# Kernel optimization log

Measured on AMD Instinct MI355X. Metric: run time of the kernel, lower is better.

## Reference

```python
import jax, jax.numpy as jnp
import numpy as np
from jax import lax

N_NEURONS = 2500
K = 50
T = 60
F = 5
H = 128
GROUP_SIZES = [800, 700, 600, 400]  # support_resistance, trend, pattern, volume
GID = jnp.asarray(np.repeat(np.arange(4), GROUP_SIZES))  # [N] specialty id per neuron
_BOUNDS = np.cumsum([0] + GROUP_SIZES)


def _lstm_layer(x, w_ih, w_hh, b_ih, b_hh):
    # x: [B,T,in]; PyTorch gate order i,f,g,o in the 4H weight rows
    B = x.shape[0]
    Hd = w_hh.shape[1]
    def step(carry, xt):
        h, c = carry
        g = xt @ w_ih.T + h @ w_hh.T + b_ih + b_hh
        i, f, gg, o = jnp.split(g, 4, axis=-1)
        c = jax.nn.sigmoid(f) * c + jax.nn.sigmoid(i) * jnp.tanh(gg)
        h = jax.nn.sigmoid(o) * jnp.tanh(c)
        return (h, c), h
    init = (jnp.zeros((B, Hd), x.dtype), jnp.zeros((B, Hd), x.dtype))
    (h, _), ys = lax.scan(step, init, jnp.swapaxes(x, 0, 1))
    return jnp.swapaxes(ys, 0, 1), h


def _forward(x, w_ih0, w_hh0, b_ih0, b_hh0, w_ih1, w_hh1, b_ih1, b_hh1,
             pw1, pb1, pw2, pb2, conn_w, sens, thr,
             iw1, ib1, iw2, ib2, iw3, ib3,
             hw_trend, hb_trend, hw_pat, hb_pat, hw_key, hb_key,
             hw_vol, hb_vol, hw_conf, hb_conf, conn_idx):
    seq, _ = _lstm_layer(x, w_ih0, w_hh0, b_ih0, b_hh0)
    _, h2 = _lstm_layer(seq, w_ih1, w_hh1, b_ih1, b_hh1)  # hidden[-1]: [B,H]
    # feature_projection: Linear->ReLU->Linear->Tanh
    base = jnp.tanh(jax.nn.relu(h2 @ pw1.T + pb1) @ pw2.T + pb2)  # [B,32]
    # broadcast base features to a per-neuron activation vector [B,N]
    reps = -(-N_NEURONS // base.shape[1])
    all_act = jnp.tile(base, (1, reps))[:, :N_NEURONS]
    # batched sparse gather + per-neuron weighted sum
    gathered = all_act[:, conn_idx]                       # [B,N,K]
    z = jnp.einsum('bnk,nk->bn', gathered, conn_w) * sens  # [B,N]
    # specialty-conditioned activation
    a = jnp.where(GID == 0, jax.nn.sigmoid(z - thr),
        jnp.where(GID == 1, jnp.tanh(z),
        jnp.where(GID == 2, jax.nn.relu(z - thr), jax.nn.sigmoid(z))))
    # integrator (dropout is eval-mode no-op)
    integ = jnp.tanh(jax.nn.relu(jax.nn.relu(a @ iw1.T + ib1) @ iw2.T + ib2) @ iw3.T + ib3)
    trend = integ @ hw_trend.T + hb_trend      # [B,3]
    pat = integ @ hw_pat.T + hb_pat            # [B,6]
    key_l = integ @ hw_key.T + hb_key          # [B,4]
    vol = integ @ hw_vol.T + hb_vol            # [B,1]
    conf = integ @ hw_conf.T + hb_conf         # [B,1]
    overall = jax.nn.sigmoid(conf)             # [B,1]
    means = jnp.stack([a[:, _BOUNDS[i]:_BOUNDS[i + 1]].mean(axis=1) for i in range(4)], axis=1)
    return jnp.concatenate([trend, pat, key_l, vol, conf, overall, means], axis=1)  # [B,20]


def setup_inputs() -> dict:
    key = jax.random.key(0)
    ks = iter(jax.random.split(key, 64))
    def rn(shape, s=0.05):
        return jax.random.normal(next(ks), shape, jnp.float32) * s
    B = 1024
    return {
        'x': jax.random.normal(next(ks), (B, T, F), jnp.float32),
        'conn_idx': jax.random.randint(next(ks), (N_NEURONS, K), 0, N_NEURONS, jnp.int32),
        'w_ih0': rn((4 * H, F)), 'w_hh0': rn((4 * H, H)),
        'b_ih0': rn((4 * H,), 0.01), 'b_hh0': rn((4 * H,), 0.01),
        'w_ih1': rn((4 * H, H)), 'w_hh1': rn((4 * H, H)),
        'b_ih1': rn((4 * H,), 0.01), 'b_hh1': rn((4 * H,), 0.01),
        'pw1': rn((64, H)), 'pb1': rn((64,), 0.01),
        'pw2': rn((32, 64)), 'pb2': rn((32,), 0.01),
        'conn_w': rn((N_NEURONS, K), 0.1),
        'sens': rn((N_NEURONS,), 0.1) + 1.0,
        'thr': rn((N_NEURONS,), 0.1) + 0.6,
        'iw1': rn((256, N_NEURONS), 0.01), 'ib1': rn((256,), 0.01),
        'iw2': rn((64, 256)), 'ib2': rn((64,), 0.01),
        'iw3': rn((32, 64)), 'ib3': rn((32,), 0.01),
        'hw_trend': rn((3, 32)), 'hb_trend': rn((3,), 0.01),
        'hw_pat': rn((6, 32)), 'hb_pat': rn((6,), 0.01),
        'hw_key': rn((4, 32)), 'hb_key': rn((4,), 0.01),
        'hw_vol': rn((1, 32)), 'hb_vol': rn((1,), 0.01),
        'hw_conf': rn((1, 32)), 'hb_conf': rn((1,), 0.01),
    }


def reference(x, conn_idx, w_ih0, w_hh0, b_ih0, b_hh0, w_ih1, w_hh1, b_ih1, b_hh1,
              pw1, pb1, pw2, pb2, conn_w, sens, thr,
              iw1, ib1, iw2, ib2, iw3, ib3,
              hw_trend, hb_trend, hw_pat, hb_pat, hw_key, hb_key,
              hw_vol, hb_vol, hw_conf, hb_conf):
    return _forward(x, w_ih0, w_hh0, b_ih0, b_hh0, w_ih1, w_hh1, b_ih1, b_hh1,
                    pw1, pb1, pw2, pb2, conn_w, sens, thr,
                    iw1, ib1, iw2, ib2, iw3, ib3,
                    hw_trend, hb_trend, hw_pat, hb_pat, hw_key, hb_key,
                    hw_vol, hb_vol, hw_conf, hb_conf, conn_idx)
```

## Files before the change

kernel.cpp:

```cpp
#include <hip/hip_runtime.h>
#include <hip/hip_bf16.h>
#include <math.h>

#define DEV __device__ __forceinline__

typedef short short8 __attribute__((ext_vector_type(8)));
typedef float f32x4  __attribute__((ext_vector_type(4)));

DEV float sigf(float x)   { return 1.0f / (1.0f + __expf(-x)); }
DEV float tanhft(float x) { return 1.0f - 2.0f / (__expf(2.0f * x) + 1.0f); }

DEV unsigned short f2bf(float f) {
    unsigned int u = __float_as_uint(f);
    unsigned int r = (u + 0x7FFFu + ((u >> 16) & 1u)) >> 16;
    return (unsigned short)r;
}
DEV float bf2f(unsigned short u) {
    return __uint_as_float(((unsigned int)u) << 16);
}

DEV void bar_lds() {
    asm volatile("s_waitcnt lgkmcnt(0)" ::: "memory");
    __builtin_amdgcn_s_barrier();
}

__global__ __launch_bounds__(256) void prep_kernel(
    const float* __restrict__ w_hh0, const float* __restrict__ w_ih1,
    const float* __restrict__ w_hh1,
    const float* __restrict__ b_ih0, const float* __restrict__ b_hh0,
    const float* __restrict__ b_ih1, const float* __restrict__ b_hh1,
    unsigned short* __restrict__ whh0h, unsigned short* __restrict__ wih1h,
    unsigned short* __restrict__ whh1h,
    float* __restrict__ bias0, float* __restrict__ bias1)
{
    int i = blockIdx.x * 256 + threadIdx.x;
    if (i < 65536) {
        whh0h[i] = f2bf(w_hh0[i]);
        wih1h[i] = f2bf(w_ih1[i]);
        whh1h[i] = f2bf(w_hh1[i]);
    } else if (i < 66048) {
        int c = i - 65536;
        bias0[c] = b_ih0[c] + b_hh0[c];
        bias1[c] = b_ih1[c] + b_hh1[c];
    }
}

__global__ __launch_bounds__(256) void prep_iw1_kernel(
    const float* __restrict__ iw1, unsigned short* __restrict__ iw1b)
{
    int i = blockIdx.x * 256 + threadIdx.x;
    if (i < 256 * 2528) {
        int row = i / 2528, k = i - row * 2528;
        iw1b[i] = (k < 2500) ? f2bf(iw1[row * 2500 + k]) : (unsigned short)0;
    }
}

__global__ __launch_bounds__(512, 2) void lstm_kernel(
    const float* __restrict__ x,
    const unsigned short* __restrict__ whh0,
    const unsigned short* __restrict__ wih1,
    const unsigned short* __restrict__ whh1,
    const float* __restrict__ wih0,
    const float* __restrict__ bias0, const float* __restrict__ bias1,
    float* __restrict__ h2out)
{
    __shared__ __align__(16) float          xs[4][304];
    __shared__ __align__(16) unsigned short h0s[2][16][136];
    __shared__ __align__(16) unsigned short h1s[2][16][136];
    __shared__ __align__(16) float          wsc[8][4][16][4];
    __shared__ float wih0s[2560];

    const int tid = threadIdx.x;
    const int b0  = blockIdx.x * 4;
    const int l15 = tid & 15;
    const int q   = (tid >> 4) & 3;
    const int w   = tid >> 6;
    const int j   = w * 16 + l15;
    const int q8  = q * 8;

    for (int i = tid; i < 1200; i += 512) {
        int m = i / 300, kk = i - m * 300;
        xs[m][kk] = x[(b0 + m) * 300 + kk];
    }
    for (int i = tid; i < 2560; i += 512) wih0s[i] = wih0[i];
    for (int i = tid; i < 2176; i += 512) {
        ((unsigned int*)h0s)[i] = 0u;
        ((unsigned int*)h1s)[i] = 0u;
    }

    float ub0[4], ub1[4];
#pragma unroll
    for (int g = 0; g < 4; ++g) {
        ub0[g] = bias0[g * 128 + j];
        ub1[g] = bias1[g * 128 + j];
    }

    short8 bh0[4][4], b1i[4][4];
#pragma unroll
    for (int g = 0; g < 4; ++g)
#pragma unroll
        for (int kc = 0; kc < 4; ++kc) {
            int off = (g * 128 + j) * 128 + kc * 32 + q8;
            bh0[g][kc] = *(const short8*)(whh0 + off);
            b1i[g][kc] = *(const short8*)(wih1 + off);
        }

    float c0 = 0.f, c1 = 0.f, hl = 0.f;
    __syncthreads();

    const unsigned short* wsb = whh1 + j * 128 + q8;

    for (int t = 0; t < 60; ++t) {
        const int p = t & 1;

        short8 wsv[4][4];
#pragma unroll
        for (int g = 0; g < 4; ++g) {
            wsv[g][0] = *(const short8*)(wsb + g * 16384);
            wsv[g][1] = *(const short8*)(wsb + g * 16384 + 32);
        }

        f32x4 acc[4];
#pragma unroll
        for (int g = 0; g < 4; ++g) acc[g] = (f32x4){0.f, 0.f, 0.f, 0.f};
        short8 af[4];
#pragma unroll
        for (int kc = 0; kc < 4; ++kc)
            af[kc] = *(const short8*)&h0s[p][l15][kc * 32 + q8];
#pragma unroll
        for (int kc = 0; kc < 4; ++kc)
#pragma unroll
            for (int g = 0; g < 4; ++g)
                acc[g] = __builtin_amdgcn_mfma_f32_16x16x32_bf16(af[kc], bh0[g][kc], acc[g], 0, 0, 0);

#pragma unroll
        for (int g = 0; g < 4; ++g) {
            wsv[g][2] = *(const short8*)(wsb + g * 16384 + 64);
            wsv[g][3] = *(const short8*)(wsb + g * 16384 + 96);
        }

        if (q == 0) {
#pragma unroll
            for (int g = 0; g < 4; ++g)
                *(f32x4*)&wsc[w][g][l15][0] = acc[g];
        }
        {
            const float* xr = &xs[q][t * 5];
            float x0 = xr[0], x1 = xr[1], x2 = xr[2], x3 = xr[3], x4 = xr[4];
            float gv[4];
#pragma unroll
            for (int g = 0; g < 4; ++g) {
                const float* wr = &wih0s[(g * 128 + j) * 5];
                float s = wsc[w][g][l15][q] + ub0[g];
                s = fmaf(x0, wr[0], s);
                s = fmaf(x1, wr[1], s);
                s = fmaf(x2, wr[2], s);
                s = fmaf(x3, wr[3], s);
                gv[g] = fmaf(x4, wr[4], s);
            }
            c0 = sigf(gv[1]) * c0 + sigf(gv[0]) * tanhft(gv[2]);
            float h = sigf(gv[3]) * tanhft(c0);
            h0s[1 - p][q][j] = f2bf(h);
        }

        bar_lds();

#pragma unroll
        for (int g = 0; g < 4; ++g) acc[g] = (f32x4){0.f, 0.f, 0.f, 0.f};
#pragma unroll
        for (int kc = 0; kc < 4; ++kc)
            af[kc] = *(const short8*)&h0s[1 - p][l15][kc * 32 + q8];
#pragma unroll
        for (int kc = 0; kc < 4; ++kc)
#pragma unroll
            for (int g = 0; g < 4; ++g)
                acc[g] = __builtin_amdgcn_mfma_f32_16x16x32_bf16(af[kc], b1i[g][kc], acc[g], 0, 0, 0);
#pragma unroll
        for (int kc = 0; kc < 4; ++kc)
            af[kc] = *(const short8*)&h1s[p][l15][kc * 32 + q8];
#pragma unroll
        for (int kc = 0; kc < 4; ++kc)
#pragma unroll
            for (int g = 0; g < 4; ++g)
                acc[g] = __builtin_amdgcn_mfma_f32_16x16x32_bf16(af[kc], wsv[g][kc], acc[g], 0, 0, 0);

        if (q == 0) {
#pragma unroll
            for (int g = 0; g < 4; ++g)
                *(f32x4*)&wsc[w][g][l15][0] = acc[g];
        }
        {
            float gv[4];
#pragma unroll
            for (int g = 0; g < 4; ++g)
                gv[g] = wsc[w][g][l15][q] + ub1[g];
            c1 = sigf(gv[1]) * c1 + sigf(gv[0]) * tanhft(gv[2]);
            float h = sigf(gv[3]) * tanhft(c1);
            h1s[1 - p][q][j] = f2bf(h);
            hl = h;
        }
    }

    h2out[(b0 + q) * 128 + j] = hl;
}

__global__ __launch_bounds__(64) void phase2_kernel(
    const float* __restrict__ h2, const float* __restrict__ pw1,
    const float* __restrict__ pb1, const float* __restrict__ pw2,
    const float* __restrict__ pb2, float* __restrict__ base)
{
    __shared__ float hs[128], p1[64];
    int b = blockIdx.x, tid = threadIdx.x;
    hs[tid] = h2[b * 128 + tid];
    hs[tid + 64] = h2[b * 128 + 64 + tid];
    __syncthreads();
    float acc = pb1[tid];
#pragma unroll 4
    for (int k = 0; k < 128; ++k) acc = fmaf(hs[k], pw1[tid * 128 + k], acc);
    p1[tid] = fmaxf(acc, 0.f);
    __syncthreads();
    if (tid < 32) {
        float a2 = pb2[tid];
#pragma unroll 4
        for (int k = 0; k < 64; ++k) a2 = fmaf(p1[k], pw2[tid * 64 + k], a2);
        base[b * 32 + tid] = tanhft(a2);
    }
}

__global__ __launch_bounds__(128) void weff_kernel(
    const int* __restrict__ conn_idx, const float* __restrict__ conn_w,
    float* __restrict__ weffT)
{
    __shared__ float s[128 * 33];
    int tid = threadIdx.x;
    int n = blockIdx.x * 128 + tid;
    float* sr = &s[tid * 33];
#pragma unroll
    for (int j = 0; j < 32; ++j) sr[j] = 0.f;
    if (n < 2500) {
        for (int k = 0; k < 50; ++k) {
            int idx = conn_idx[n * 50 + k];
            sr[idx & 31] += conn_w[n * 50 + k];
        }
        for (int j = 0; j < 32; ++j) weffT[j * 2500 + n] = sr[j];
    }
}

__global__ __launch_bounds__(256) void za_kernel(
    const float* __restrict__ base, const float* __restrict__ weffT,
    const float* __restrict__ sens, const float* __restrict__ thr,
    unsigned short* __restrict__ amat)
{
    __shared__ float bs[16][32];
    int tid = threadIdx.x;
    int bb = blockIdx.x / 10, nb = blockIdx.x % 10;
    int n = nb * 256 + tid;
    bool nv = n < 2500;
    bool pv = n < 2528;
    int nn = nv ? n : 0;
    for (int i = tid; i < 512; i += 256) bs[i >> 5][i & 31] = base[bb * 512 + i];
    __syncthreads();
    float w[32];
#pragma unroll
    for (int j = 0; j < 32; ++j) w[j] = weffT[j * 2500 + nn];
    float sn = sens[nn], tn = thr[nn];
    int g = (n < 800) ? 0 : (n < 1500) ? 1 : (n < 2100) ? 2 : 3;
#pragma unroll 2
    for (int r = 0; r < 16; ++r) {
        float z = 0.f;
#pragma unroll
        for (int j = 0; j < 32; ++j) z = fmaf(bs[r][j], w[j], z);
        z *= sn;
        float av;
        if (g == 0)      av = sigf(z - tn);
        else if (g == 1) av = tanhft(z);
        else if (g == 2) av = fmaxf(z - tn, 0.f);
        else             av = sigf(z);
        if (nv)      amat[(bb * 16 + r) * 2528 + n] = f2bf(av);
        else if (pv) amat[(bb * 16 + r) * 2528 + n] = 0;
    }
}

__global__ __launch_bounds__(128) void gemm_iw1_kernel(
    const unsigned short* __restrict__ ab, const unsigned short* __restrict__ wb,
    const float* __restrict__ ib1, float* __restrict__ t1)
{
    const int tid = threadIdx.x;
    const int wv  = tid >> 6;
    const int l15 = tid & 15, q = (tid >> 4) & 3, q8 = q * 8;
    const int row0 = blockIdx.y * 32 + wv * 16;
    const int col0 = blockIdx.x * 64;

    const unsigned short* A = ab + (row0 + l15) * 2528 + q8;
    const unsigned short* B = wb + (col0 + l15) * 2528 + q8;

    short8 a = *(const short8*)A;
    short8 b[4];
#pragma unroll
    for (int nt = 0; nt < 4; ++nt) b[nt] = *(const short8*)(B + nt * 16 * 2528);

    f32x4 acc[4];
#pragma unroll
    for (int nt = 0; nt < 4; ++nt) acc[nt] = (f32x4){0.f, 0.f, 0.f, 0.f};

    for (int c = 0; c < 79; ++c) {
        int cn = (c < 78) ? c + 1 : 78;
        short8 an = *(const short8*)(A + cn * 32);
        short8 bn[4];
#pragma unroll
        for (int nt = 0; nt < 4; ++nt)
            bn[nt] = *(const short8*)(B + nt * 16 * 2528 + cn * 32);
#pragma unroll
        for (int nt = 0; nt < 4; ++nt)
            acc[nt] = __builtin_amdgcn_mfma_f32_16x16x32_bf16(a, b[nt], acc[nt], 0, 0, 0);
        a = an;
#pragma unroll
        for (int nt = 0; nt < 4; ++nt) b[nt] = bn[nt];
    }

#pragma unroll
    for (int nt = 0; nt < 4; ++nt) {
        int n = col0 + nt * 16 + l15;
        float bias = ib1[n];
#pragma unroll
        for (int i = 0; i < 4; ++i) {
            int row = row0 + q * 4 + i;
            t1[row * 256 + n] = fmaxf(acc[nt][i] + bias, 0.f);
        }
    }
}

__global__ __launch_bounds__(64) void final_kernel(
    const float* __restrict__ t1, const float* __restrict__ iw2,
    const float* __restrict__ ib2, const float* __restrict__ iw3,
    const float* __restrict__ ib3,
    const float* __restrict__ hw_trend, const float* __restrict__ hb_trend,
    const float* __restrict__ hw_pat,   const float* __restrict__ hb_pat,
    const float* __restrict__ hw_key,   const float* __restrict__ hb_key,
    const float* __restrict__ hw_vol,   const float* __restrict__ hb_vol,
    const float* __restrict__ hw_conf,  const float* __restrict__ hb_conf,
    float* __restrict__ out)
{
    __shared__ float t1s[256], t2s[64], igs[32];
    int b = blockIdx.x, tid = threadIdx.x;
#pragma unroll
    for (int i = 0; i < 4; ++i) t1s[tid + i * 64] = t1[b * 256 + tid + i * 64];
    __syncthreads();
    float acc = ib2[tid];
#pragma unroll 4
    for (int k = 0; k < 256; ++k) acc = fmaf(t1s[k], iw2[tid * 256 + k], acc);
    t2s[tid] = fmaxf(acc, 0.f);
    __syncthreads();
    if (tid < 32) {
        float a2 = ib3[tid];
#pragma unroll 4
        for (int k = 0; k < 64; ++k) a2 = fmaf(t2s[k], iw3[tid * 64 + k], a2);
        igs[tid] = tanhft(a2);
    }
    __syncthreads();
    if (tid < 15) {
        const float* w; const float* bb; int j, off;
        if (tid < 3)        { w = hw_trend; bb = hb_trend; j = tid;     off = 0; }
        else if (tid < 9)   { w = hw_pat;   bb = hb_pat;   j = tid - 3; off = 3; }
        else if (tid < 13)  { w = hw_key;   bb = hb_key;   j = tid - 9; off = 9; }
        else if (tid == 13) { w = hw_vol;   bb = hb_vol;   j = 0;       off = 13; }
        else                { w = hw_conf;  bb = hb_conf;  j = 0;       off = 14; }
        float a3 = bb[j];
#pragma unroll
        for (int k = 0; k < 32; ++k) a3 = fmaf(igs[k], w[j * 32 + k], a3);
        out[b * 20 + off + j] = a3;
        if (tid == 14) out[b * 20 + 15] = sigf(a3);
    }
}

__global__ __launch_bounds__(256) void means_kernel(
    const unsigned short* __restrict__ amat, float* __restrict__ out)
{
    __shared__ float red[16];
    int b = blockIdx.x, tid = threadIdx.x;
    float parts[4] = {0.f, 0.f, 0.f, 0.f};
    for (int n0 = tid * 8; n0 < 2500; n0 += 2048) {
        short8 v = *(const short8*)(amat + b * 2528 + n0);
#pragma unroll
        for (int e = 0; e < 8; ++e) {
            int n = n0 + e;
            float f = bf2f((unsigned short)v[e]);
            if (n < 800)       parts[0] += f;
            else if (n < 1500) parts[1] += f;
            else if (n < 2100) parts[2] += f;
            else               parts[3] += f;
        }
    }
    int lane = tid & 63, wv = tid >> 6;
#pragma unroll
    for (int g = 0; g < 4; ++g) {
        float v = parts[g];
        for (int s = 32; s > 0; s >>= 1) v += __shfl_down(v, s, 64);
        if (lane == 0) red[wv * 4 + g] = v;
    }
    __syncthreads();
    if (tid < 4) {
        float s = red[tid] + red[4 + tid] + red[8 + tid] + red[12 + tid];
        float invg = (tid == 0) ? (1.f / 800.f) : (tid == 1) ? (1.f / 700.f)
                   : (tid == 2) ? (1.f / 600.f) : (1.f / 400.f);
        out[b * 20 + 16 + tid] = s * invg;
    }
}

extern "C" void kernel_launch(void* const* d_in, const int* in_sizes, int n_in,
                              void* d_out, int out_size, void* d_ws, size_t ws_size,
                              hipStream_t stream)
{
    const float* x        = (const float*)d_in[0];
    const int*   conn_idx = (const int*)  d_in[1];
    const float* w_ih0    = (const float*)d_in[2];
    const float* w_hh0    = (const float*)d_in[3];
    const float* b_ih0    = (const float*)d_in[4];
    const float* b_hh0    = (const float*)d_in[5];
    const float* w_ih1    = (const float*)d_in[6];
    const float* w_hh1    = (const float*)d_in[7];
    const float* b_ih1    = (const float*)d_in[8];
    const float* b_hh1    = (const float*)d_in[9];
    const float* pw1      = (const float*)d_in[10];
    const float* pb1      = (const float*)d_in[11];
    const float* pw2      = (const float*)d_in[12];
    const float* pb2      = (const float*)d_in[13];
    const float* conn_w   = (const float*)d_in[14];
    const float* sens     = (const float*)d_in[15];
    const float* thr      = (const float*)d_in[16];
    const float* iw1      = (const float*)d_in[17];
    const float* ib1      = (const float*)d_in[18];
    const float* iw2      = (const float*)d_in[19];
    const float* ib2      = (const float*)d_in[20];
    const float* iw3      = (const float*)d_in[21];
    const float* ib3      = (const float*)d_in[22];
    const float* hw_trend = (const float*)d_in[23];
    const float* hb_trend = (const float*)d_in[24];
    const float* hw_pat   = (const float*)d_in[25];
    const float* hb_pat   = (const float*)d_in[26];
    const float* hw_key   = (const float*)d_in[27];
    const float* hb_key   = (const float*)d_in[28];
    const float* hw_vol   = (const float*)d_in[29];
    const float* hb_vol   = (const float*)d_in[30];
    const float* hw_conf  = (const float*)d_in[31];
    const float* hb_conf  = (const float*)d_in[32];
    float* out = (float*)d_out;
    float* ws  = (float*)d_ws;

    unsigned short* whh0h = (unsigned short*)(ws);
    unsigned short* wih1h = (unsigned short*)(ws + 32768);
    unsigned short* whh1h = (unsigned short*)(ws + 65536);
    float* bias0  = ws + 98304;
    float* bias1  = ws + 98816;
    float* h2     = ws + 99328;
    float* base_  = ws + 230400;
    float* weffT  = ws + 263168;
    float* t1     = ws + 343168;
    unsigned short* iw1b   = (unsigned short*)(ws + 605312);
    unsigned short* amatbf = (unsigned short*)(ws + 928896);

    prep_kernel<<<258, 256, 0, stream>>>(w_hh0, w_ih1, w_hh1,
                                         b_ih0, b_hh0, b_ih1, b_hh1,
                                         whh0h, wih1h, whh1h, bias0, bias1);
    prep_iw1_kernel<<<2528, 256, 0, stream>>>(iw1, iw1b);
    lstm_kernel<<<256, 512, 0, stream>>>(x, whh0h, wih1h, whh1h, w_ih0,
                                         bias0, bias1, h2);
    phase2_kernel<<<1024, 64, 0, stream>>>(h2, pw1, pb1, pw2, pb2, base_);
    weff_kernel<<<20, 128, 0, stream>>>(conn_idx, conn_w, weffT);
    za_kernel<<<640, 256, 0, stream>>>(base_, weffT, sens, thr, amatbf);
    gemm_iw1_kernel<<<dim3(4, 32), 128, 0, stream>>>(amatbf, iw1b, ib1, t1);
    final_kernel<<<1024, 64, 0, stream>>>(t1, iw2, ib2, iw3, ib3,
                                          hw_trend, hb_trend, hw_pat, hb_pat,
                                          hw_key, hb_key, hw_vol, hb_vol,
                                          hw_conf, hb_conf, out);
    means_kernel<<<1024, 256, 0, stream>>>(amatbf, out);
}
```

Before: 316.3 us.

## Stage MLP weights in LDS across four rows and narrow iw1 GEMM tiles

phase2 and final kernels now each process four batch rows per 256-thread block. They stage the pw1/pw2 and iw2/iw3 weight matrices in padded shared memory so each block reuses them instead of rereading global weights per row. The iw1 GEMM tile width is halved to 32 columns, which doubles the grid to 256 blocks for better occupancy on many CUs, at the cost of more A-matrix rereads. The weight staging adds a large per-block LDS copy (about 66KB in final_kernel), which may limit occupancy.

```diff
diff --git a/kernel.cpp b/kernel.cpp
--- a/kernel.cpp
+++ b/kernel.cpp
@@ -204,26 +204,50 @@
     h2out[(b0 + q) * 128 + j] = hl;
 }
 
-__global__ __launch_bounds__(64) void phase2_kernel(
+__global__ __launch_bounds__(256) void phase2_kernel(
     const float* __restrict__ h2, const float* __restrict__ pw1,
     const float* __restrict__ pb1, const float* __restrict__ pw2,
     const float* __restrict__ pb2, float* __restrict__ base)
 {
-    __shared__ float hs[128], p1[64];
-    int b = blockIdx.x, tid = threadIdx.x;
-    hs[tid] = h2[b * 128 + tid];
-    hs[tid + 64] = h2[b * 128 + 64 + tid];
-    __syncthreads();
-    float acc = pb1[tid];
+    __shared__ float pw1s[64 * 129];
+    __shared__ float pw2s[32 * 65];
+    __shared__ float hs[4][128];
+    __shared__ float p1s[4][64];
+
+    const int tid = threadIdx.x;
+    const int b0  = blockIdx.x * 4;
+
+    for (int i = tid; i < 8192; i += 256) {
+        int u = i >> 7, k = i & 127;
+        pw1s[u * 129 + k] = pw1[i];
+    }
+    for (int i = tid; i < 2048; i += 256) {
+        int u = i >> 6, k = i & 63;
+        pw2s[u * 65 + k] = pw2[i];
+    }
+    for (int i = tid; i < 512; i += 256)
+        hs[i >> 7][i & 127] = h2[b0 * 128 + i];
+    __syncthreads();
+
+    {
+        const int r = tid >> 6, u = tid & 63;
+        float acc = pb1[u];
+        const float* wr = &pw1s[u * 129];
+        const float* hr = &hs[r][0];
 #pragma unroll 4
-    for (int k = 0; k < 128; ++k) acc = fmaf(hs[k], pw1[tid * 128 + k], acc);
-    p1[tid] = fmaxf(acc, 0.f);
-    __syncthreads();
-    if (tid < 32) {
-        float a2 = pb2[tid];
+        for (int k = 0; k < 128; ++k) acc = fmaf(hr[k], wr[k], acc);
+        p1s[r][u] = fmaxf(acc, 0.f);
+    }
+    __syncthreads();
+
+    if (tid < 128) {
+        const int r = tid >> 5, u2 = tid & 31;
+        float a2 = pb2[u2];
+        const float* wr = &pw2s[u2 * 65];
+        const float* pr = &p1s[r][0];
 #pragma unroll 4
-        for (int k = 0; k < 64; ++k) a2 = fmaf(p1[k], pw2[tid * 64 + k], a2);
-        base[b * 32 + tid] = tanhft(a2);
+        for (int k = 0; k < 64; ++k) a2 = fmaf(pr[k], wr[k], a2);
+        base[(b0 + r) * 32 + u2] = tanhft(a2);
     }
 }
 
@@ -289,37 +313,37 @@
     const int wv  = tid >> 6;
     const int l15 = tid & 15, q = (tid >> 4) & 3, q8 = q * 8;
     const int row0 = blockIdx.y * 32 + wv * 16;
-    const int col0 = blockIdx.x * 64;
+    const int col0 = blockIdx.x * 32;
 
     const unsigned short* A = ab + (row0 + l15) * 2528 + q8;
     const unsigned short* B = wb + (col0 + l15) * 2528 + q8;
 
     short8 a = *(const short8*)A;
-    short8 b[4];
-#pragma unroll
-    for (int nt = 0; nt < 4; ++nt) b[nt] = *(const short8*)(B + nt * 16 * 2528);
-
-    f32x4 acc[4];
-#pragma unroll
-    for (int nt = 0; nt < 4; ++nt) acc[nt] = (f32x4){0.f, 0.f, 0.f, 0.f};
+    short8 b[2];
+#pragma unroll
+    for (int nt = 0; nt < 2; ++nt) b[nt] = *(const short8*)(B + nt * 16 * 2528);
+
+    f32x4 acc[2];
+#pragma unroll
+    for (int nt = 0; nt < 2; ++nt) acc[nt] = (f32x4){0.f, 0.f, 0.f, 0.f};
 
     for (int c = 0; c < 79; ++c) {
         int cn = (c < 78) ? c + 1 : 78;
         short8 an = *(const short8*)(A + cn * 32);
-        short8 bn[4];
-#pragma unroll
-        for (int nt = 0; nt < 4; ++nt)
+        short8 bn[2];
+#pragma unroll
+        for (int nt = 0; nt < 2; ++nt)
             bn[nt] = *(const short8*)(B + nt * 16 * 2528 + cn * 32);
 #pragma unroll
-        for (int nt = 0; nt < 4; ++nt)
+        for (int nt = 0; nt < 2; ++nt)
             acc[nt] = __builtin_amdgcn_mfma_f32_16x16x32_bf16(a, b[nt], acc[nt], 0, 0, 0);
         a = an;
 #pragma unroll
-        for (int nt = 0; nt < 4; ++nt) b[nt] = bn[nt];
-    }
-
-#pragma unroll
-    for (int nt = 0; nt < 4; ++nt) {
+        for (int nt = 0; nt < 2; ++nt) b[nt] = bn[nt];
+    }
+
+#pragma unroll
+    for (int nt = 0; nt < 2; ++nt) {
         int n = col0 + nt * 16 + l15;
         float bias = ib1[n];
 #pragma unroll
@@ -330,7 +354,7 @@
     }
 }
 
-__global__ __launch_bounds__(64) void final_kernel(
+__global__ __launch_bounds__(256) void final_kernel(
     const float* __restrict__ t1, const float* __restrict__ iw2,
     const float* __restrict__ ib2, const float* __restrict__ iw3,
     const float* __restrict__ ib3,
@@ -341,35 +365,63 @@
     const float* __restrict__ hw_conf,  const float* __restrict__ hb_conf,
     float* __restrict__ out)
 {
-    __shared__ float t1s[256], t2s[64], igs[32];
-    int b = blockIdx.x, tid = threadIdx.x;
-#pragma unroll
-    for (int i = 0; i < 4; ++i) t1s[tid + i * 64] = t1[b * 256 + tid + i * 64];
-    __syncthreads();
-    float acc = ib2[tid];
+    __shared__ float iw2s[64 * 257];
+    __shared__ float iw3s[32 * 65];
+    __shared__ float t1s[4][256];
+    __shared__ float t2s[4][64];
+    __shared__ float igs[4][32];
+
+    const int tid = threadIdx.x;
+    const int b0  = blockIdx.x * 4;
+
+    for (int i = tid; i < 16384; i += 256) {
+        int u = i >> 8, k = i & 255;
+        iw2s[u * 257 + k] = iw2[i];
+    }
+    for (int i = tid; i < 2048; i += 256) {
+        int u = i >> 6, k = i & 63;
+        iw3s[u * 65 + k] = iw3[i];
+    }
+    for (int i = tid; i < 1024; i += 256)
+        t1s[i >> 8][i & 255] = t1[b0 * 256 + i];
+    __syncthreads();
+
+    {
+        const int r = tid >> 6, u = tid & 63;
+        float acc = ib2[u];
+        const float* wr = &iw2s[u * 257];
+        const float* tr = &t1s[r][0];
 #pragma unroll 4
-    for (int k = 0; k < 256; ++k) acc = fmaf(t1s[k], iw2[tid * 256 + k], acc);
-    t2s[tid] = fmaxf(acc, 0.f);
-    __syncthreads();
-    if (tid < 32) {
-        float a2 = ib3[tid];
+        for (int k = 0; k < 256; ++k) acc = fmaf(tr[k], wr[k], acc);
+        t2s[r][u] = fmaxf(acc, 0.f);
+    }
+    __syncthreads();
+
+    if (tid < 128) {
+        const int r = tid >> 5, u2 = tid & 31;
+        float a2 = ib3[u2];
+        const float* wr = &iw3s[u2 * 65];
+        const float* tr = &t2s[r][0];
 #pragma unroll 4
-        for (int k = 0; k < 64; ++k) a2 = fmaf(t2s[k], iw3[tid * 64 + k], a2);
-        igs[tid] = tanhft(a2);
-    }
-    __syncthreads();
-    if (tid < 15) {
+        for (int k = 0; k < 64; ++k) a2 = fmaf(tr[k], wr[k], a2);
+        igs[r][u2] = tanhft(a2);
+    }
+    __syncthreads();
+
+    if (tid < 60) {
+        const int r = tid / 15, t15 = tid % 15;
+        const int b = b0 + r;
         const float* w; const float* bb; int j, off;
-        if (tid < 3)        { w = hw_trend; bb = hb_trend; j = tid;     off = 0; }
-        else if (tid < 9)   { w = hw_pat;   bb = hb_pat;   j = tid - 3; off = 3; }
-        else if (tid < 13)  { w = hw_key;   bb = hb_key;   j = tid - 9; off = 9; }
-        else if (tid == 13) { w = hw_vol;   bb = hb_vol;   j = 0;       off = 13; }
+        if (t15 < 3)        { w = hw_trend; bb = hb_trend; j = t15;     off = 0; }
+        else if (t15 < 9)   { w = hw_pat;   bb = hb_pat;   j = t15 - 3; off = 3; }
+        else if (t15 < 13)  { w = hw_key;   bb = hb_key;   j = t15 - 9; off = 9; }
+        else if (t15 == 13) { w = hw_vol;   bb = hb_vol;   j = 0;       off = 13; }
         else                { w = hw_conf;  bb = hb_conf;  j = 0;       off = 14; }
         float a3 = bb[j];
 #pragma unroll
-        for (int k = 0; k < 32; ++k) a3 = fmaf(igs[k], w[j * 32 + k], a3);
+        for (int k = 0; k < 32; ++k) a3 = fmaf(igs[r][k], w[j * 32 + k], a3);
         out[b * 20 + off + j] = a3;
-        if (tid == 14) out[b * 20 + 15] = sigf(a3);
+        if (t15 == 14) out[b * 20 + 15] = sigf(a3);
     }
 }
 
@@ -465,11 +517,11 @@
     prep_iw1_kernel<<<2528, 256, 0, stream>>>(iw1, iw1b);
     lstm_kernel<<<256, 512, 0, stream>>>(x, whh0h, wih1h, whh1h, w_ih0,
                                          bias0, bias1, h2);
-    phase2_kernel<<<1024, 64, 0, stream>>>(h2, pw1, pb1, pw2, pb2, base_);
+    phase2_kernel<<<256, 256, 0, stream>>>(h2, pw1, pb1, pw2, pb2, base_);
     weff_kernel<<<20, 128, 0, stream>>>(conn_idx, conn_w, weffT);
     za_kernel<<<640, 256, 0, stream>>>(base_, weffT, sens, thr, amatbf);
-    gemm_iw1_kernel<<<dim3(4, 32), 128, 0, stream>>>(amatbf, iw1b, ib1, t1);
-    final_kernel<<<1024, 64, 0, stream>>>(t1, iw2, ib2, iw3, ib3,
+    gemm_iw1_kernel<<<dim3(8, 32), 128, 0, stream>>>(amatbf, iw1b, ib1, t1);
+    final_kernel<<<256, 256, 0, stream>>>(t1, iw2, ib2, iw3, ib3,
                                           hw_trend, hb_trend, hw_pat, hb_pat,
                                           hw_key, hb_key, hw_vol, hb_vol,
                                           hw_conf, hb_conf, out);
```

Result: faster. 294.9 us (-6.8%).
